# Kernel optimization log

Hardware: AMD Instinct MI355X
Metric: run time of the kernel (lower is better)

Reference implementation:

```python
import jax, jax.numpy as jnp
import numpy as np

B, N, E = 4, 10000, 100000
C_IN = 16              # 16x0e input scalars
N_EDGE_FEAT = 128
MUL0, MUL1 = 16, 8     # out_irreps = 16x0e + 8x1o -> dim 16 + 24 = 40
W_NUMEL = C_IN * MUL0 + C_IN * MUL1  # 384
MODES = 2
OUT_DIM = MUL0 + 3 * MUL1
ALPHA = 1.0 / np.sqrt(float(C_IN))   # e3nn element path normalization (fan_in = mul_in*mul_sh = 16)
BN_EPS = 1e-5


def setup_inputs() -> dict:
    key = jax.random.key(0)
    ks = jax.random.split(key, 12)
    x = jax.random.normal(ks[0], (B, N, C_IN), jnp.float32)
    edge_index = jax.random.randint(ks[1], (2, E), 0, N)
    edge_attr = jax.random.normal(ks[2], (B, E, N_EDGE_FEAT), jnp.float32)
    edge_sh = jax.random.normal(ks[3], (B, E, 4), jnp.float32)
    scale = 1.0 / (C_IN * MUL0)
    tc_wr = scale * jax.random.uniform(ks[4], (C_IN, MUL0, MODES), jnp.float32)
    tc_wi = scale * jax.random.uniform(ks[5], (C_IN, MUL0, MODES), jnp.float32)
    mlp_w1 = jax.random.normal(ks[6], (N_EDGE_FEAT, N_EDGE_FEAT), jnp.float32) / np.sqrt(N_EDGE_FEAT)
    mlp_b1 = jnp.zeros((N_EDGE_FEAT,), jnp.float32)
    mlp_w2 = jax.random.normal(ks[7], (N_EDGE_FEAT, W_NUMEL), jnp.float32) / np.sqrt(N_EDGE_FEAT)
    mlp_b2 = jnp.zeros((W_NUMEL,), jnp.float32)
    bn_gamma = jnp.ones((OUT_DIM,), jnp.float32)
    bn_beta = jnp.zeros((OUT_DIM,), jnp.float32)
    return dict(x=x, edge_index=edge_index, edge_attr=edge_attr, edge_sh=edge_sh,
                tc_wr=tc_wr, tc_wi=tc_wi, mlp_w1=mlp_w1, mlp_b1=mlp_b1,
                mlp_w2=mlp_w2, mlp_b2=mlp_b2, bn_gamma=bn_gamma, bn_beta=bn_beta)


def reference(x, edge_index, edge_attr, edge_sh, tc_wr, tc_wi,
              mlp_w1, mlp_b1, mlp_w2, mlp_b2, bn_gamma, bn_beta):
    Bx, Nx, _ = x.shape
    # --- SimplifiedSpectralConv1d over the batch (time) axis ---
    n_fft = min(8, Bx)
    W = tc_wr + 1j * tc_wi                       # [C_IN, MUL0, MODES] complex64
    x_ft = jnp.fft.rfft(x, n=n_fft, axis=0)      # [n_fft//2+1, N, C_IN]
    out_ft = jnp.zeros((x_ft.shape[0], Nx, MUL0), dtype=x_ft.dtype)
    out_ft = out_ft.at[:MODES].set(jnp.einsum('bni,iom->bno', x_ft[:MODES], W))
    xs = jnp.fft.irfft(out_ft, n=n_fft, axis=0)
    if xs.shape[0] < Bx:
        xs = jnp.pad(xs, ((0, Bx - xs.shape[0]), (0, 0), (0, 0)))
    x = xs[:Bx]                                   # [B, N, MUL0] (scalar block fully replaced)

    # --- per-edge weights from edge MLP ---
    h = jax.nn.relu(edge_attr @ mlp_w1 + mlp_b1)
    ew = h @ mlp_w2 + mlp_b2                      # [B, E, 384]
    w1 = ew[..., :C_IN * MUL0].reshape(Bx, E, C_IN, MUL0)
    w2 = ew[..., C_IN * MUL0:].reshape(Bx, E, C_IN, MUL1)

    # --- gather + fully connected tensor product (0e x 0e -> 0e, 0e x 1o -> 1o) ---
    src, dst = edge_index[0], edge_index[1]
    xg = x[:, src]                                # [B, E, C_IN]
    sh0 = edge_sh[..., 0]                         # [B, E]
    sh1 = edge_sh[..., 1:4]                       # [B, E, 3]
    out0 = jnp.einsum('bei,beio->beo', xg * sh0[..., None], w1) * ALPHA          # [B,E,16]
    out1 = (jnp.einsum('bei,beio,bem->beom', xg, w2, sh1) * ALPHA).reshape(Bx, E, 3 * MUL1)
    msg = jnp.concatenate([out0, out1], axis=-1)  # [B, E, 40]

    # --- scatter-mean into destination nodes ---
    seg_sum = jax.vmap(lambda m: jax.ops.segment_sum(m, dst, num_segments=Nx))(msg)
    cnt = jax.ops.segment_sum(jnp.ones((E,), msg.dtype), dst, num_segments=Nx)
    agg = seg_sum / jnp.maximum(cnt, 1.0)[None, :, None]   # [B, N, 40]

    # --- BatchNorm1d (training-mode batch statistics) over flattened B*N ---
    flat = agg.reshape(-1, OUT_DIM)
    mu = flat.mean(axis=0)
    var = flat.var(axis=0)
    out = (agg - mu) * jax.lax.rsqrt(var + BN_EPS) * bn_gamma + bn_beta
    return out
```

## Files before the change

kernel.cpp:

```cpp
#include <hip/hip_runtime.h>

#define B_CNT 4
#define N_CNT 10000
#define E_CNT 100000

typedef __attribute__((ext_vector_type(8))) short s16x8;
typedef __attribute__((ext_vector_type(4))) float f32x4;

__device__ __forceinline__ float b2f(unsigned short u) {
  union { unsigned int i; float f; } v; v.i = ((unsigned int)u) << 16; return v.f;
}
__device__ __forceinline__ unsigned short f2b(float f) {
  union { float f; unsigned int i; } v; v.f = f;
  unsigned int b = v.i;
  b += 0x7FFFu + ((b >> 16) & 1u);
  return (unsigned short)(b >> 16);
}
__device__ __forceinline__ short f2bs(float f) { return (short)f2b(f); }

__global__ void k_fft(const float* __restrict__ x,
                      const float* __restrict__ tcwr,
                      const float* __restrict__ tcwi,
                      float* __restrict__ xnew) {
  __shared__ float Wr[256], Wi[256];
  const int t = threadIdx.x;
  Wr[t] = tcwr[t * 2] + tcwr[t * 2 + 1];
  Wi[t] = tcwi[t * 2] + tcwi[t * 2 + 1];
  __syncthreads();
  const int n = blockIdx.x * 256 + t;
  if (n >= N_CNT) return;

  float xt[4][16];
  for (int tt = 0; tt < 4; ++tt) {
    const float* xp = x + ((size_t)tt * N_CNT + n) * 16;
#pragma unroll
    for (int i0 = 0; i0 < 16; i0 += 4) {
      const float4 v = *(const float4*)(xp + i0);
      xt[tt][i0 + 0] = v.x; xt[tt][i0 + 1] = v.y;
      xt[tt][i0 + 2] = v.z; xt[tt][i0 + 3] = v.w;
    }
  }
  float s[16], a[16], bb[16];
#pragma unroll
  for (int i = 0; i < 16; ++i) {
    s[i]  = xt[0][i] + xt[1][i] + xt[2][i] + xt[3][i];
    a[i]  = xt[0][i] - xt[2][i];
    bb[i] = xt[1][i] - xt[3][i];
  }
  for (int o = 0; o < 16; ++o) {
    float r0 = 0.f, p = 0.f, qq = 0.f;
#pragma unroll
    for (int i = 0; i < 16; ++i) {
      const float wr = Wr[i * 16 + o], wi = Wi[i * 16 + o];
      r0 += s[i] * wr;
      p  += a[i] * wr + bb[i] * wi;
      qq += a[i] * wi - bb[i] * wr;
    }
    xnew[((size_t)0 * N_CNT + n) * 16 + o] = 0.25f * (r0 + 2.f * p);
    xnew[((size_t)1 * N_CNT + n) * 16 + o] = 0.25f * (r0 - 2.f * qq);
    xnew[((size_t)2 * N_CNT + n) * 16 + o] = 0.25f * (r0 - 2.f * p);
    xnew[((size_t)3 * N_CNT + n) * 16 + o] = 0.25f * (r0 + 2.f * qq);
  }
}

__global__ void k_pack(const float* __restrict__ w1,
                       const float* __restrict__ w2,
                       unsigned short* __restrict__ pw1,
                       unsigned short* __restrict__ pw2) {
  const int t = blockIdx.x * 256 + threadIdx.x;
  const int tile = t >> 6, l = t & 63, q = l >> 4, lm = l & 15;
  if (tile < 32) {
    const int nt = tile >> 2, kk = tile & 3;
    const int n = nt * 16 + lm;
    unsigned short* dst = pw1 + ((size_t)tile * 64 + l) * 8;
#pragma unroll
    for (int j = 0; j < 8; ++j) dst[j] = f2b(w1[(kk * 32 + q * 8 + j) * 128 + n]);
  } else {
    const int t2 = tile - 32;
    const int nt = t2 >> 2, kk = t2 & 3;
    int col;
    if (nt < 16) col = nt * 16 + lm;
    else col = 256 + (8 * (lm & 1) + (nt - 16)) * 8 + (lm >> 1);
    unsigned short* dst = pw2 + ((size_t)t2 * 64 + l) * 8;
#pragma unroll
    for (int j = 0; j < 8; ++j) dst[j] = f2b(w2[(kk * 32 + q * 8 + j) * 384 + col]);
  }
}

__global__ void k_cnt(const int* __restrict__ eidx, int* __restrict__ cnt) {
  const int e = blockIdx.x * 256 + threadIdx.x;
  if (e < E_CNT) atomicAdd(&cnt[eidx[E_CNT + e]], 1);
}

__global__ void k_scan(const int* __restrict__ cnt, int* __restrict__ rowstart,
                       int* __restrict__ runoff) {
  __shared__ int partial[256];
  const int t = threadIdx.x;
  const int c0 = t * 40;
  int s = 0;
  for (int j = 0; j < 40; ++j) {
    const int idx = c0 + j;
    if (idx < N_CNT) s += cnt[idx];
  }
  partial[t] = s;
  __syncthreads();
  if (t == 0) {
    int acc = 0;
    for (int i = 0; i < 256; ++i) { const int v = partial[i]; partial[i] = acc; acc += v; }
  }
  __syncthreads();
  int acc = partial[t];
  for (int j = 0; j < 40; ++j) {
    const int idx = c0 + j;
    if (idx < N_CNT) { rowstart[idx] = acc; runoff[idx] = acc; acc += cnt[idx]; }
  }
  if (t == 255) rowstart[N_CNT] = acc;
}

__global__ void k_pos(const int* __restrict__ eidx, int* __restrict__ runoff,
                      int* __restrict__ pos) {
  const int e = blockIdx.x * 256 + threadIdx.x;
  if (e < E_CNT) pos[e] = atomicAdd(&runoff[eidx[E_CNT + e]], 1);
}

template <bool ATOMIC>
__global__ __launch_bounds__(256, 4) void k_edge(
    const float* __restrict__ ea, const int* __restrict__ eidx,
    const float* __restrict__ esh,
    const unsigned short* __restrict__ pw1, const unsigned short* __restrict__ pw2,
    const float* __restrict__ b1v, const float* __restrict__ b2v,
    const float* __restrict__ xnew, const int* __restrict__ idx_arr,
    float* __restrict__ out_base, const size_t bstride) {
  __shared__ __align__(16) unsigned short Hs[32 * 136];
  __shared__ __align__(16) unsigned short EWt[32 * 392];
  __shared__ float xgs[32 * 20];
  __shared__ float shs[32 * 4];
  __shared__ int ids[32];

  const int t = threadIdx.x;
  const int b = blockIdx.y;
  const int e0 = blockIdx.x * 32;
  const int w = t >> 6, l = t & 63, q = l >> 4, lm = l & 15;

  if (t < 128) {
    const int el = t >> 2, i0 = (t & 3) * 4;
    const int src = eidx[e0 + el];
    const float4 v = *(const float4*)(xnew + ((size_t)b * N_CNT + src) * 16 + i0);
    xgs[el * 20 + i0 + 0] = v.x;
    xgs[el * 20 + i0 + 1] = v.y;
    xgs[el * 20 + i0 + 2] = v.z;
    xgs[el * 20 + i0 + 3] = v.w;
  } else if (t < 160) {
    const int el = t - 128;
    const float4 v = *(const float4*)(esh + ((size_t)b * E_CNT + e0 + el) * 4);
    shs[el * 4 + 0] = v.x;
    shs[el * 4 + 1] = v.y;
    shs[el * 4 + 2] = v.z;
    shs[el * 4 + 3] = v.w;
  } else if (t < 192) {
    const int el = t - 160;
    ids[el] = idx_arr[e0 + el];
  }

  f32x4 acc1[2][2];
#pragma unroll
  for (int mt = 0; mt < 2; ++mt)
#pragma unroll
    for (int j = 0; j < 2; ++j) acc1[mt][j] = (f32x4)0.0f;

  const float* eab = ea + (size_t)b * E_CNT * 128;
  float4 araw[4][2][2];
#pragma unroll
  for (int kk = 0; kk < 4; ++kk)
#pragma unroll
    for (int mt = 0; mt < 2; ++mt) {
      const float* ap = eab + ((size_t)(e0 + mt * 16 + lm)) * 128 + kk * 32 + q * 8;
      araw[kk][mt][0] = *(const float4*)ap;
      araw[kk][mt][1] = *(const float4*)(ap + 4);
    }
#pragma unroll
  for (int kk = 0; kk < 4; ++kk) {
    const s16x8 bf0 = *(const s16x8*)(pw1 + (((size_t)(2 * w + 0) * 4 + kk) * 64 + l) * 8);
    const s16x8 bf1 = *(const s16x8*)(pw1 + (((size_t)(2 * w + 1) * 4 + kk) * 64 + l) * 8);
#pragma unroll
    for (int mt = 0; mt < 2; ++mt) {
      const float4 a0 = araw[kk][mt][0];
      const float4 a1 = araw[kk][mt][1];
      const s16x8 af = { f2bs(a0.x), f2bs(a0.y), f2bs(a0.z), f2bs(a0.w),
                         f2bs(a1.x), f2bs(a1.y), f2bs(a1.z), f2bs(a1.w) };
      acc1[mt][0] = __builtin_amdgcn_mfma_f32_16x16x32_bf16(af, bf0, acc1[mt][0], 0, 0, 0);
      acc1[mt][1] = __builtin_amdgcn_mfma_f32_16x16x32_bf16(af, bf1, acc1[mt][1], 0, 0, 0);
    }
  }
#pragma unroll
  for (int j = 0; j < 2; ++j) {
    const int n = (2 * w + j) * 16 + lm;
    const float bias = b1v[n];
#pragma unroll
    for (int mt = 0; mt < 2; ++mt)
#pragma unroll
      for (int r = 0; r < 4; ++r) {
        float v = acc1[mt][j][r] + bias;
        v = fmaxf(v, 0.0f);
        Hs[(mt * 16 + q * 4 + r) * 136 + n] = f2b(v);
      }
  }

  s16x8 bw0[6];
#pragma unroll
  for (int jj = 0; jj < 6; ++jj)
    bw0[jj] = *(const s16x8*)(pw2 + (((size_t)(6 * w + jj) * 4 + 0) * 64 + l) * 8);
  __syncthreads();

  f32x4 acc2[2][6];
#pragma unroll
  for (int mt = 0; mt < 2; ++mt)
#pragma unroll
    for (int jj = 0; jj < 6; ++jj) acc2[mt][jj] = (f32x4)0.0f;

#pragma unroll
  for (int kk = 0; kk < 4; ++kk) {
    s16x8 bw[6];
    if (kk == 0) {
#pragma unroll
      for (int jj = 0; jj < 6; ++jj) bw[jj] = bw0[jj];
    } else {
#pragma unroll
      for (int jj = 0; jj < 6; ++jj)
        bw[jj] = *(const s16x8*)(pw2 + (((size_t)(6 * w + jj) * 4 + kk) * 64 + l) * 8);
    }
#pragma unroll
    for (int mt = 0; mt < 2; ++mt) {
      const s16x8 ah = *(const s16x8*)(&Hs[(mt * 16 + lm) * 136 + kk * 32 + q * 8]);
#pragma unroll
      for (int jj = 0; jj < 6; ++jj)
        acc2[mt][jj] = __builtin_amdgcn_mfma_f32_16x16x32_bf16(ah, bw[jj], acc2[mt][jj], 0, 0, 0);
    }
  }

  float bias6[6];
#pragma unroll
  for (int jj = 0; jj < 6; ++jj) {
    const int T = 6 * w + jj;
    const int bcol = (T < 16) ? (T * 16 + lm)
                              : (256 + (8 * (l & 1) + (T - 16)) * 8 + (lm >> 1));
    bias6[jj] = b2v[bcol];
  }
#pragma unroll
  for (int mt = 0; mt < 2; ++mt)
#pragma unroll
    for (int r = 0; r < 4; ++r) {
      const int edge = mt * 16 + q * 4 + r;
      unsigned short u[6];
#pragma unroll
      for (int jj = 0; jj < 6; ++jj) u[jj] = f2b(acc2[mt][jj][r] + bias6[jj]);
      const unsigned int p0 = (unsigned int)u[0] | ((unsigned int)u[1] << 16);
      const unsigned int p1 = (unsigned int)u[2] | ((unsigned int)u[3] << 16);
      const unsigned int p2 = (unsigned int)u[4] | ((unsigned int)u[5] << 16);
      unsigned int* base = (unsigned int*)&EWt[edge * 392];
      if (w < 2) {
        unsigned int* d = base + lm * 8 + 3 * w;
        d[0] = p0; d[1] = p1; d[2] = p2;
      } else if (w == 2) {
        unsigned int* d = base + lm * 8 + 6;
        d[0] = p0; d[1] = p1;
        base[(16 + (lm >> 1)) * 8 + 4 * (l & 1)] = p2;
      } else {
        unsigned int* d = base + (16 + (lm >> 1)) * 8 + 4 * (l & 1) + 1;
        d[0] = p0; d[1] = p1; d[2] = p2;
      }
    }
  __syncthreads();

  {
    const int m = t >> 3, sub = t & 7;
    float xr[16];
#pragma unroll
    for (int i0 = 0; i0 < 16; i0 += 4) {
      const float4 v = *(const float4*)&xgs[m * 20 + i0];
      xr[i0] = v.x; xr[i0 + 1] = v.y; xr[i0 + 2] = v.z; xr[i0 + 3] = v.w;
    }
    const float sh0v = 0.25f * shs[m * 4 + 0];
    const float s1a = 0.25f * shs[m * 4 + 1];
    const float s1b = 0.25f * shs[m * 4 + 2];
    const float s1c = 0.25f * shs[m * 4 + 3];
    float* outp = out_base + (size_t)b * bstride + (size_t)ids[m] * 40;
#pragma unroll
    for (int dd = 0; dd < 3; ++dd) {
      const int d = sub * 3 + dd;
      const unsigned short* ep = &EWt[m * 392 + d * 16];
      const s16x8 eA = *(const s16x8*)ep;
      const s16x8 eB = *(const s16x8*)(ep + 8);
      float dotv = 0.f;
#pragma unroll
      for (int i = 0; i < 8; ++i) {
        dotv += xr[i] * b2f((unsigned short)eA[i]);
        dotv += xr[8 + i] * b2f((unsigned short)eB[i]);
      }
      if (d < 16) {
        const float val = dotv * sh0v;
        if (ATOMIC) atomicAdd(outp + d, val); else outp[d] = val;
      } else {
        const int c0 = 16 + (d - 16) * 3;
        if (ATOMIC) {
          atomicAdd(outp + c0 + 0, dotv * s1a);
          atomicAdd(outp + c0 + 1, dotv * s1b);
          atomicAdd(outp + c0 + 2, dotv * s1c);
        } else {
          outp[c0 + 0] = dotv * s1a;
          outp[c0 + 1] = dotv * s1b;
          outp[c0 + 2] = dotv * s1c;
        }
      }
    }
  }
}

__global__ void k_agg(float* __restrict__ sums, const int* __restrict__ cnt,
                      float* __restrict__ psum, float* __restrict__ psq) {
  __shared__ float ls[40], lq[40];
  const int t = threadIdx.x;
  if (t < 40) { ls[t] = 0.f; lq[t] = 0.f; }
  __syncthreads();
  const unsigned base = blockIdx.x * 2048u + t;
  for (int k2 = 0; k2 < 8; ++k2) {
    const unsigned idx = base + k2 * 256u;
    if (idx < 1600000u) {
      const unsigned row = idx / 40u;
      const unsigned node = row % 10000u;
      const float c = (float)cnt[node];
      const float v = sums[idx] / fmaxf(c, 1.f);
      sums[idx] = v;
      const unsigned ch = idx - row * 40u;
      atomicAdd(&ls[ch], v);
      atomicAdd(&lq[ch], v * v);
    }
  }
  __syncthreads();
  if (t < 40) {
    atomicAdd(&psum[t], ls[t]);
    atomicAdd(&psq[t], lq[t]);
  }
}

__global__ __launch_bounds__(256) void k_gather(
    const float* __restrict__ msgbuf, const int* __restrict__ rowstart,
    float* __restrict__ sums, float* __restrict__ psum, float* __restrict__ psq) {
  const int t = threadIdx.x;
  const int wid = t >> 6, ch = t & 63;
  float lsum = 0.f, lsq = 0.f;
  for (int k = 0; k < 16; ++k) {
    const int p = blockIdx.x * 64 + wid * 16 + k;
    const int bb = p / 10000;
    const int node = p - bb * 10000;
    const int r0 = rowstart[node], r1 = rowstart[node + 1];
    if (ch < 40) {
      float v = 0.f;
      for (int r = r0; r < r1; ++r) v += msgbuf[((size_t)bb * E_CNT + r) * 40 + ch];
      v /= fmaxf((float)(r1 - r0), 1.f);
      sums[(size_t)p * 40 + ch] = v;
      lsum += v; lsq += v * v;
    }
  }
  if (ch < 40) {
    atomicAdd(&psum[ch], lsum);
    atomicAdd(&psq[ch], lsq);
  }
}

__global__ void k_stats(const float* __restrict__ psum, const float* __restrict__ psq,
                        const float* __restrict__ gma, const float* __restrict__ bta,
                        float* __restrict__ scalev, float* __restrict__ shiftv) {
  const int t = threadIdx.x;
  if (t < 40) {
    const float inv = 1.0f / 40000.0f;
    const float mu = psum[t] * inv;
    const float var = psq[t] * inv - mu * mu;
    const float sc = rsqrtf(fmaxf(var, 0.0f) + 1e-5f) * gma[t];
    scalev[t] = sc;
    shiftv[t] = bta[t] - mu * sc;
  }
}

__global__ void k_out(const float* __restrict__ agg, const float* __restrict__ scalev,
                      const float* __restrict__ shiftv, float* __restrict__ outp) {
  __shared__ float sc[40], sh[40];
  const int t = threadIdx.x;
  if (t < 40) { sc[t] = scalev[t]; sh[t] = shiftv[t]; }
  __syncthreads();
  const unsigned base = blockIdx.x * 1024u + t;
#pragma unroll
  for (int k2 = 0; k2 < 4; ++k2) {
    const unsigned idx = base + k2 * 256u;
    if (idx < 1600000u) {
      const unsigned row = idx / 40u;
      const unsigned ch = idx - row * 40u;
      outp[idx] = agg[idx] * sc[ch] + sh[ch];
    }
  }
}

extern "C" void kernel_launch(void* const* d_in, const int* in_sizes, int n_in,
                              void* d_out, int out_size, void* d_ws, size_t ws_size,
                              hipStream_t stream) {
  (void)in_sizes; (void)n_in; (void)out_size;
  const float* x    = (const float*)d_in[0];
  const int*   eidx = (const int*)d_in[1];
  const float* ea   = (const float*)d_in[2];
  const float* esh  = (const float*)d_in[3];
  const float* tcwr = (const float*)d_in[4];
  const float* tcwi = (const float*)d_in[5];
  const float* w1   = (const float*)d_in[6];
  const float* b1   = (const float*)d_in[7];
  const float* w2   = (const float*)d_in[8];
  const float* b2   = (const float*)d_in[9];
  const float* gma  = (const float*)d_in[10];
  const float* bta  = (const float*)d_in[11];

  char* ws = (char*)d_ws;
  float*          sums     = (float*)(ws + 0);
  int*            cnt      = (int*)(ws + 6400000);
  float*          psum     = (float*)(ws + 6440000);
  float*          psq      = (float*)(ws + 6440160);
  float*          xnew     = (float*)(ws + 6440448);
  unsigned short* pw1      = (unsigned short*)(ws + 9000448);
  unsigned short* pw2      = (unsigned short*)(ws + 9033216);
  float*          scalev   = (float*)(ws + 9131520);
  float*          shiftv   = (float*)(ws + 9131680);
  int*            rowstart = (int*)(ws + 9131840);
  int*            runoff   = (int*)(ws + 9171856);
  int*            pos      = (int*)(ws + 9211856);
  float*          msgbuf   = (float*)(ws + 9611904);

  const bool use_csr = ws_size >= (size_t)73611904;

  if (use_csr) {
    hipMemsetAsync(ws + 6400000, 0, 40320, stream);
    k_fft<<<dim3(40), dim3(256), 0, stream>>>(x, tcwr, tcwi, xnew);
    k_pack<<<dim3(32), dim3(256), 0, stream>>>(w1, w2, pw1, pw2);
    k_cnt<<<dim3(391), dim3(256), 0, stream>>>(eidx, cnt);
    k_scan<<<dim3(1), dim3(256), 0, stream>>>(cnt, rowstart, runoff);
    k_pos<<<dim3(391), dim3(256), 0, stream>>>(eidx, runoff, pos);
    k_edge<false><<<dim3(E_CNT / 32, B_CNT), dim3(256), 0, stream>>>(
        ea, eidx, esh, pw1, pw2, b1, b2, xnew, pos, msgbuf, (size_t)E_CNT * 40);
    k_gather<<<dim3(625), dim3(256), 0, stream>>>(msgbuf, rowstart, sums, psum, psq);
    k_stats<<<dim3(1), dim3(64), 0, stream>>>(psum, psq, gma, bta, scalev, shiftv);
    k_out<<<dim3(1563), dim3(256), 0, stream>>>(sums, scalev, shiftv, (float*)d_out);
  } else {
    hipMemsetAsync(ws, 0, 6440320, stream);
    k_fft<<<dim3(40), dim3(256), 0, stream>>>(x, tcwr, tcwi, xnew);
    k_pack<<<dim3(32), dim3(256), 0, stream>>>(w1, w2, pw1, pw2);
    k_cnt<<<dim3(391), dim3(256), 0, stream>>>(eidx, cnt);
    k_edge<true><<<dim3(E_CNT / 32, B_CNT), dim3(256), 0, stream>>>(
        ea, eidx, esh, pw1, pw2, b1, b2, xnew, eidx + E_CNT, sums, (size_t)N_CNT * 40);
    k_agg<<<dim3(782), dim3(256), 0, stream>>>(sums, cnt, psum, psq);
    k_stats<<<dim3(1), dim3(64), 0, stream>>>(psum, psq, gma, bta, scalev, shiftv);
    k_out<<<dim3(1563), dim3(256), 0, stream>>>(sums, scalev, shiftv, (float*)d_out);
  }
}
```

Measured before the change: 627.2 us.

## Use packed bf16 converts, swizzle LDS stores, unroll gather, fuse stats into output

Replaces the software float-to-bf16 rounding with the hardware v_cvt_pk_bf16_f32 instruction in the MLP stages. All first-layer weight fragments are hoisted and loaded early, with empty asm keep-alives to force those loads to issue before the MFMAs. EWt stores and loads are XOR-swizzled by quad parity to reduce LDS bank conflicts. The CSR gather now uses four independent accumulators, launches twice as many smaller blocks and returns idle lanes early. The single-block stats kernel is folded into k_out, so every output block recomputes scale and shift, saving a launch at the cost of a little redundant work.

```diff
diff --git a/kernel.cpp b/kernel.cpp
--- a/kernel.cpp
+++ b/kernel.cpp
@@ -6,6 +6,7 @@
 
 typedef __attribute__((ext_vector_type(8))) short s16x8;
 typedef __attribute__((ext_vector_type(4))) float f32x4;
+typedef __attribute__((ext_vector_type(4))) unsigned int u32x4;
 
 __device__ __forceinline__ float b2f(unsigned short u) {
   union { unsigned int i; float f; } v; v.i = ((unsigned int)u) << 16; return v.f;
@@ -16,7 +17,18 @@
   b += 0x7FFFu + ((b >> 16) & 1u);
   return (unsigned short)(b >> 16);
 }
-__device__ __forceinline__ short f2bs(float f) { return (short)f2b(f); }
+__device__ __forceinline__ unsigned int cvtpk(float lo, float hi) {
+  unsigned int r;
+  asm("v_cvt_pk_bf16_f32 %0, %1, %2" : "=v"(r) : "v"(lo), "v"(hi));
+  return r;
+}
+__device__ __forceinline__ void keepf4(const float4& v) {
+  asm volatile("" :: "v"(v.x), "v"(v.y), "v"(v.z), "v"(v.w));
+}
+__device__ __forceinline__ void keeps(s16x8 v) {
+  u32x4 u = __builtin_bit_cast(u32x4, v);
+  asm volatile("" :: "v"(u.x), "v"(u.y), "v"(u.z), "v"(u.w));
+}
 
 __global__ void k_fft(const float* __restrict__ x,
                       const float* __restrict__ tcwr,
@@ -162,12 +174,6 @@
     ids[el] = idx_arr[e0 + el];
   }
 
-  f32x4 acc1[2][2];
-#pragma unroll
-  for (int mt = 0; mt < 2; ++mt)
-#pragma unroll
-    for (int j = 0; j < 2; ++j) acc1[mt][j] = (f32x4)0.0f;
-
   const float* eab = ea + (size_t)b * E_CNT * 128;
   float4 araw[4][2][2];
 #pragma unroll
@@ -178,38 +184,65 @@
       araw[kk][mt][0] = *(const float4*)ap;
       araw[kk][mt][1] = *(const float4*)(ap + 4);
     }
+  s16x8 bfr[2][4];
+#pragma unroll
+  for (int j = 0; j < 2; ++j)
+#pragma unroll
+    for (int kk = 0; kk < 4; ++kk)
+      bfr[j][kk] = *(const s16x8*)(pw1 + (((size_t)(2 * w + j) * 4 + kk) * 64 + l) * 8);
+#pragma unroll
+  for (int kk = 0; kk < 4; ++kk)
+#pragma unroll
+    for (int mt = 0; mt < 2; ++mt) { keepf4(araw[kk][mt][0]); keepf4(araw[kk][mt][1]); }
+#pragma unroll
+  for (int j = 0; j < 2; ++j)
+#pragma unroll
+    for (int kk = 0; kk < 4; ++kk) keeps(bfr[j][kk]);
+
+  f32x4 acc1[2][2];
+#pragma unroll
+  for (int mt = 0; mt < 2; ++mt)
+#pragma unroll
+    for (int j = 0; j < 2; ++j) acc1[mt][j] = (f32x4)0.0f;
+
 #pragma unroll
   for (int kk = 0; kk < 4; ++kk) {
-    const s16x8 bf0 = *(const s16x8*)(pw1 + (((size_t)(2 * w + 0) * 4 + kk) * 64 + l) * 8);
-    const s16x8 bf1 = *(const s16x8*)(pw1 + (((size_t)(2 * w + 1) * 4 + kk) * 64 + l) * 8);
 #pragma unroll
     for (int mt = 0; mt < 2; ++mt) {
       const float4 a0 = araw[kk][mt][0];
       const float4 a1 = araw[kk][mt][1];
-      const s16x8 af = { f2bs(a0.x), f2bs(a0.y), f2bs(a0.z), f2bs(a0.w),
-                         f2bs(a1.x), f2bs(a1.y), f2bs(a1.z), f2bs(a1.w) };
-      acc1[mt][0] = __builtin_amdgcn_mfma_f32_16x16x32_bf16(af, bf0, acc1[mt][0], 0, 0, 0);
-      acc1[mt][1] = __builtin_amdgcn_mfma_f32_16x16x32_bf16(af, bf1, acc1[mt][1], 0, 0, 0);
-    }
-  }
+      union { unsigned int u[4]; s16x8 s; } au;
+      au.u[0] = cvtpk(a0.x, a0.y); au.u[1] = cvtpk(a0.z, a0.w);
+      au.u[2] = cvtpk(a1.x, a1.y); au.u[3] = cvtpk(a1.z, a1.w);
+      const s16x8 af = au.s;
+      acc1[mt][0] = __builtin_amdgcn_mfma_f32_16x16x32_bf16(af, bfr[0][kk], acc1[mt][0], 0, 0, 0);
+      acc1[mt][1] = __builtin_amdgcn_mfma_f32_16x16x32_bf16(af, bfr[1][kk], acc1[mt][1], 0, 0, 0);
+    }
+  }
+
+  s16x8 bw0[6];
+#pragma unroll
+  for (int jj = 0; jj < 6; ++jj)
+    bw0[jj] = *(const s16x8*)(pw2 + (((size_t)(6 * w + jj) * 4 + 0) * 64 + l) * 8);
+
 #pragma unroll
   for (int j = 0; j < 2; ++j) {
     const int n = (2 * w + j) * 16 + lm;
     const float bias = b1v[n];
 #pragma unroll
-    for (int mt = 0; mt < 2; ++mt)
-#pragma unroll
-      for (int r = 0; r < 4; ++r) {
-        float v = acc1[mt][j][r] + bias;
-        v = fmaxf(v, 0.0f);
-        Hs[(mt * 16 + q * 4 + r) * 136 + n] = f2b(v);
+    for (int mt = 0; mt < 2; ++mt) {
+#pragma unroll
+      for (int r = 0; r < 4; r += 2) {
+        const float v0 = fmaxf(acc1[mt][j][r] + bias, 0.0f);
+        const float v1 = fmaxf(acc1[mt][j][r + 1] + bias, 0.0f);
+        const unsigned int pr = cvtpk(v0, v1);
+        Hs[(mt * 16 + q * 4 + r) * 136 + n] = (unsigned short)pr;
+        Hs[(mt * 16 + q * 4 + r + 1) * 136 + n] = (unsigned short)(pr >> 16);
       }
-  }
-
-  s16x8 bw0[6];
-#pragma unroll
-  for (int jj = 0; jj < 6; ++jj)
-    bw0[jj] = *(const s16x8*)(pw2 + (((size_t)(6 * w + jj) * 4 + 0) * 64 + l) * 8);
+    }
+  }
+#pragma unroll
+  for (int jj = 0; jj < 6; ++jj) keeps(bw0[jj]);
   __syncthreads();
 
   f32x4 acc2[2][6];
@@ -246,27 +279,31 @@
                               : (256 + (8 * (l & 1) + (T - 16)) * 8 + (lm >> 1));
     bias6[jj] = b2v[bcol];
   }
+  const int sq4 = (q & 1) * 4;
+  const int nsq4 = 4 - sq4;
+  const int ch2off = (16 + (lm >> 1)) * 8 + (((l & 1) ^ (q & 1)) ? 4 : 0);
 #pragma unroll
   for (int mt = 0; mt < 2; ++mt)
 #pragma unroll
     for (int r = 0; r < 4; ++r) {
       const int edge = mt * 16 + q * 4 + r;
-      unsigned short u[6];
-#pragma unroll
-      for (int jj = 0; jj < 6; ++jj) u[jj] = f2b(acc2[mt][jj][r] + bias6[jj]);
-      const unsigned int p0 = (unsigned int)u[0] | ((unsigned int)u[1] << 16);
-      const unsigned int p1 = (unsigned int)u[2] | ((unsigned int)u[3] << 16);
-      const unsigned int p2 = (unsigned int)u[4] | ((unsigned int)u[5] << 16);
+      const unsigned int p0 = cvtpk(acc2[mt][0][r] + bias6[0], acc2[mt][1][r] + bias6[1]);
+      const unsigned int p1 = cvtpk(acc2[mt][2][r] + bias6[2], acc2[mt][3][r] + bias6[3]);
+      const unsigned int p2 = cvtpk(acc2[mt][4][r] + bias6[4], acc2[mt][5][r] + bias6[5]);
       unsigned int* base = (unsigned int*)&EWt[edge * 392];
-      if (w < 2) {
-        unsigned int* d = base + lm * 8 + 3 * w;
+      if (w == 0) {
+        unsigned int* d = base + lm * 8 + sq4;
         d[0] = p0; d[1] = p1; d[2] = p2;
+      } else if (w == 1) {
+        base[lm * 8 + sq4 + 3] = p0;
+        unsigned int* d = base + lm * 8 + nsq4;
+        d[0] = p1; d[1] = p2;
       } else if (w == 2) {
-        unsigned int* d = base + lm * 8 + 6;
+        unsigned int* d = base + lm * 8 + nsq4 + 2;
         d[0] = p0; d[1] = p1;
-        base[(16 + (lm >> 1)) * 8 + 4 * (l & 1)] = p2;
+        base[ch2off] = p2;
       } else {
-        unsigned int* d = base + (16 + (lm >> 1)) * 8 + 4 * (l & 1) + 1;
+        unsigned int* d = base + ch2off + 1;
         d[0] = p0; d[1] = p1; d[2] = p2;
       }
     }
@@ -274,6 +311,7 @@
 
   {
     const int m = t >> 3, sub = t & 7;
+    const int sqr8 = ((m >> 2) & 1) << 3;
     float xr[16];
 #pragma unroll
     for (int i0 = 0; i0 < 16; i0 += 4) {
@@ -289,8 +327,8 @@
     for (int dd = 0; dd < 3; ++dd) {
       const int d = sub * 3 + dd;
       const unsigned short* ep = &EWt[m * 392 + d * 16];
-      const s16x8 eA = *(const s16x8*)ep;
-      const s16x8 eB = *(const s16x8*)(ep + 8);
+      const s16x8 eA = *(const s16x8*)(ep + sqr8);
+      const s16x8 eB = *(const s16x8*)(ep + 8 - sqr8);
       float dotv = 0.f;
 #pragma unroll
       for (int i = 0; i < 8; ++i) {
@@ -348,45 +386,46 @@
     float* __restrict__ sums, float* __restrict__ psum, float* __restrict__ psq) {
   const int t = threadIdx.x;
   const int wid = t >> 6, ch = t & 63;
+  if (ch >= 40) return;
   float lsum = 0.f, lsq = 0.f;
-  for (int k = 0; k < 16; ++k) {
-    const int p = blockIdx.x * 64 + wid * 16 + k;
+  for (int k = 0; k < 8; ++k) {
+    const int p = blockIdx.x * 32 + wid * 8 + k;
     const int bb = p / 10000;
     const int node = p - bb * 10000;
     const int r0 = rowstart[node], r1 = rowstart[node + 1];
-    if (ch < 40) {
-      float v = 0.f;
-      for (int r = r0; r < r1; ++r) v += msgbuf[((size_t)bb * E_CNT + r) * 40 + ch];
-      v /= fmaxf((float)(r1 - r0), 1.f);
-      sums[(size_t)p * 40 + ch] = v;
-      lsum += v; lsq += v * v;
-    }
-  }
-  if (ch < 40) {
-    atomicAdd(&psum[ch], lsum);
-    atomicAdd(&psq[ch], lsq);
-  }
-}
-
-__global__ void k_stats(const float* __restrict__ psum, const float* __restrict__ psq,
-                        const float* __restrict__ gma, const float* __restrict__ bta,
-                        float* __restrict__ scalev, float* __restrict__ shiftv) {
+    const float* base = msgbuf + (size_t)bb * (E_CNT * 40) + ch;
+    float v0 = 0.f, v1 = 0.f, v2 = 0.f, v3 = 0.f;
+    int r = r0;
+    for (; r + 4 <= r1; r += 4) {
+      v0 += base[(size_t)(r + 0) * 40];
+      v1 += base[(size_t)(r + 1) * 40];
+      v2 += base[(size_t)(r + 2) * 40];
+      v3 += base[(size_t)(r + 3) * 40];
+    }
+    for (; r < r1; ++r) v0 += base[(size_t)r * 40];
+    float v = (v0 + v1) + (v2 + v3);
+    v /= fmaxf((float)(r1 - r0), 1.f);
+    sums[(size_t)p * 40 + ch] = v;
+    lsum += v; lsq += v * v;
+  }
+  atomicAdd(&psum[ch], lsum);
+  atomicAdd(&psq[ch], lsq);
+}
+
+__global__ void k_out(const float* __restrict__ agg,
+                      const float* __restrict__ psum, const float* __restrict__ psq,
+                      const float* __restrict__ gma, const float* __restrict__ bta,
+                      float* __restrict__ outp) {
+  __shared__ float sc[40], sh[40];
   const int t = threadIdx.x;
   if (t < 40) {
     const float inv = 1.0f / 40000.0f;
     const float mu = psum[t] * inv;
     const float var = psq[t] * inv - mu * mu;
-    const float sc = rsqrtf(fmaxf(var, 0.0f) + 1e-5f) * gma[t];
-    scalev[t] = sc;
-    shiftv[t] = bta[t] - mu * sc;
-  }
-}
-
-__global__ void k_out(const float* __restrict__ agg, const float* __restrict__ scalev,
-                      const float* __restrict__ shiftv, float* __restrict__ outp) {
-  __shared__ float sc[40], sh[40];
-  const int t = threadIdx.x;
-  if (t < 40) { sc[t] = scalev[t]; sh[t] = shiftv[t]; }
+    const float s = rsqrtf(fmaxf(var, 0.0f) + 1e-5f) * gma[t];
+    sc[t] = s;
+    sh[t] = bta[t] - mu * s;
+  }
   __syncthreads();
   const unsigned base = blockIdx.x * 1024u + t;
 #pragma unroll
@@ -425,8 +464,6 @@
   float*          xnew     = (float*)(ws + 6440448);
   unsigned short* pw1      = (unsigned short*)(ws + 9000448);
   unsigned short* pw2      = (unsigned short*)(ws + 9033216);
-  float*          scalev   = (float*)(ws + 9131520);
-  float*          shiftv   = (float*)(ws + 9131680);
   int*            rowstart = (int*)(ws + 9131840);
   int*            runoff   = (int*)(ws + 9171856);
   int*            pos      = (int*)(ws + 9211856);
@@ -443,9 +480,8 @@
     k_pos<<<dim3(391), dim3(256), 0, stream>>>(eidx, runoff, pos);
     k_edge<false><<<dim3(E_CNT / 32, B_CNT), dim3(256), 0, stream>>>(
         ea, eidx, esh, pw1, pw2, b1, b2, xnew, pos, msgbuf, (size_t)E_CNT * 40);
-    k_gather<<<dim3(625), dim3(256), 0, stream>>>(msgbuf, rowstart, sums, psum, psq);
-    k_stats<<<dim3(1), dim3(64), 0, stream>>>(psum, psq, gma, bta, scalev, shiftv);
-    k_out<<<dim3(1563), dim3(256), 0, stream>>>(sums, scalev, shiftv, (float*)d_out);
+    k_gather<<<dim3(1250), dim3(256), 0, stream>>>(msgbuf, rowstart, sums, psum, psq);
+    k_out<<<dim3(1563), dim3(256), 0, stream>>>(sums, psum, psq, gma, bta, (float*)d_out);
   } else {
     hipMemsetAsync(ws, 0, 6440320, stream);
     k_fft<<<dim3(40), dim3(256), 0, stream>>>(x, tcwr, tcwi, xnew);
@@ -454,7 +490,6 @@
     k_edge<true><<<dim3(E_CNT / 32, B_CNT), dim3(256), 0, stream>>>(
         ea, eidx, esh, pw1, pw2, b1, b2, xnew, eidx + E_CNT, sums, (size_t)N_CNT * 40);
     k_agg<<<dim3(782), dim3(256), 0, stream>>>(sums, cnt, psum, psq);
-    k_stats<<<dim3(1), dim3(64), 0, stream>>>(psum, psq, gma, bta, scalev, shiftv);
-    k_out<<<dim3(1563), dim3(256), 0, stream>>>(sums, scalev, shiftv, (float*)d_out);
-  }
-}
+    k_out<<<dim3(1563), dim3(256), 0, stream>>>(sums, psum, psq, gma, bta, (float*)d_out);
+  }
+}
```

Result: slower. 644.4 us (+2.7%).
